# Kernel tuning notes

Hardware: AMD Instinct MI355X
Metric: run time of the kernel (lower is better)

The kernel has to match this reference:

```python
import jax, jax.numpy as jnp
import numpy as np

# Reversible solver constants (init kwargs / solve args)
L = 0.999          # coupling parameter l
H = 1.0 / 64.0     # step size h
T_END = 1.0        # terminal time T
N_STEPS = int(T_END / H)  # 64 sequential steps

B, D, HID = 4096, 512, 2048


def setup_inputs() -> dict:
    key = jax.random.key(0)
    k0, k1, k2, k3 = jax.random.split(key, 4)
    s1 = 1.0 / np.sqrt(D).astype(np.float32)
    s2 = 1.0 / np.sqrt(HID).astype(np.float32)
    return {
        "y0": jax.random.normal(k0, (B, D), jnp.float32),
        "W1": jax.random.normal(k1, (D, HID), jnp.float32) * s1,
        "b1": jnp.zeros((HID,), jnp.float32),
        "wt": jax.random.normal(k2, (HID,), jnp.float32) * 0.1,
        "W2": jax.random.normal(k3, (HID, D), jnp.float32) * s2,
        "b2": jnp.zeros((D,), jnp.float32),
    }


def reference(y0, W1, b1, wt, W2, b2):
    # MLP vector field vf(t, y): [B, D] -> [B, D]
    def vf(t, y):
        hidden = jnp.tanh(y @ W1 + b1 + t * wt)  # [B, HID]
        return hidden @ W2 + b2                   # [B, D]

    # Explicit Euler solver step: step(vf, h, t, y) = h * vf(t, y)
    def euler_step(hh, t, y):
        return hh * vf(t, y)

    # Reversible forward step (faithful to _solve_forward.forward_step)
    def forward_step(carry, _):
        t0, y0_, z0 = carry
        t1 = t0 + H
        y1 = L * y0_ + (1.0 - L) * z0 + euler_step(H, t0, z0)
        z1 = z0 - euler_step(-H, t1, y1)
        return (t1, y1, z1), None

    t0 = jnp.zeros((), jnp.float32)
    (tN, yN, zN), _ = jax.lax.scan(forward_step, (t0, y0, y0), None, length=N_STEPS)
    return yN
```

## Files before the change

### kernel.cpp

```cpp
#include <hip/hip_runtime.h>
#include <hip/hip_bf16.h>

typedef __bf16 bf16x8 __attribute__((ext_vector_type(8)));
typedef float f32x4 __attribute__((ext_vector_type(4)));
typedef unsigned short u16;

#define GLD_LDS16(gp, lp) __builtin_amdgcn_global_load_lds( \
    (const __attribute__((address_space(1))) unsigned int*)(gp), \
    (__attribute__((address_space(3))) unsigned int*)(lp), 16, 0, 0)

__device__ __forceinline__ float tanh_fast(float x) {
  float e = __expf(2.0f * x);
  return 1.0f - __fdividef(2.0f, e + 1.0f);
}

__device__ __forceinline__ u16 bf16_rn(float x) {
  union { float f; unsigned u; } v; v.f = x;
  unsigned r = v.u + 0x7fffu + ((v.u >> 16) & 1u);
  return (u16)(r >> 16);
}

template <int BM, int BN, int BK, int K, int MODE, int NTL>
__global__ __launch_bounds__(256, 2)
void gemm_fused(const u16* __restrict__ A, const u16* __restrict__ Bt,
                const float* __restrict__ bias, const float* __restrict__ wt,
                float tval,
                const float* __restrict__ y_in, const float* __restrict__ z_in,
                float* __restrict__ out32, u16* __restrict__ out_bf, int N) {
  constexpr int NS = BK / 64;
  constexpr int WTM = BM / 2, WTN = BN / 2;
  constexpr int FM = WTM / 16, FN = WTN / 16;
  constexpr int ACH = BM * BK * 2 / 1024;
  constexpr int BCH = BN * BK * 2 / 1024;
  constexpr int CPS_A = BM / 8;
  constexpr int CPS_B = BN / 8;
  constexpr int MT = 4096 / BM;
  constexpr int MPX = MT / 8;
  constexpr int NCH = ACH / 4;
  static_assert(ACH / 4 == BCH / 4 || true, "");

  __shared__ u16 As[NS * BM * 64];
  __shared__ u16 Bs[NS * BN * 64];

  const int tid = threadIdx.x;
  const int wave = tid >> 6;
  const int lane = tid & 63;
  const int wm = wave >> 1, wn = wave & 1;
  const int l15 = lane & 15, kg = lane >> 4;

  const int wg = blockIdx.x;
  const int xcd = wg & 7;
  const int j = wg >> 3;
  const int bm0 = (xcd * MPX + j / NTL) * BM;
  const int bn0 = (j % NTL) * BN;

  f32x4 acc[FM][FN];
#pragma unroll
  for (int m = 0; m < FM; ++m)
#pragma unroll
    for (int n = 0; n < FN; ++n) acc[m][n] = (f32x4){0.f, 0.f, 0.f, 0.f};

  const int sr = lane >> 3;
  const int scs = ((lane & 7) ^ sr) * 8;
  const int rsw = (l15 & 7) << 3;

  const u16* Ag = A + (size_t)bm0 * K;
  const u16* Bg = Bt + (size_t)bn0 * K;

  for (int kt = 0; kt < K / BK; ++kt) {
    const u16* Ak = Ag + kt * BK;
    const u16* Bk = Bg + kt * BK;
#pragma unroll
    for (int i = 0; i < NCH; ++i) {
      {
        const int ch = wave + i * 4;
        const int kh = ch / CPS_A;
        const int rg = ch % CPS_A;
        GLD_LDS16(Ak + (size_t)(rg * 8 + sr) * K + kh * 64 + scs,
                  (char*)As + ch * 1024);
      }
      if (i < BCH / 4) {
        const int ch = wave + i * 4;
        const int kh = ch / CPS_B;
        const int rg = ch % CPS_B;
        GLD_LDS16(Bk + (size_t)(rg * 8 + sr) * K + kh * 64 + scs,
                  (char*)Bs + ch * 1024);
      }
    }
    __syncthreads();
#pragma unroll
    for (int ks = 0; ks < 2 * NS; ++ks) {
      const int kh = ks >> 1;
      const int kc = ((ks & 1) * 32 + kg * 8) ^ rsw;
      bf16x8 af[FM], bfr[FN];
#pragma unroll
      for (int m = 0; m < FM; ++m)
        af[m] = *reinterpret_cast<const bf16x8*>(
            &As[(kh * BM + wm * WTM + m * 16 + l15) * 64 + kc]);
#pragma unroll
      for (int n = 0; n < FN; ++n)
        bfr[n] = *reinterpret_cast<const bf16x8*>(
            &Bs[(kh * BN + wn * WTN + n * 16 + l15) * 64 + kc]);
      __builtin_amdgcn_s_setprio(1);
#pragma unroll
      for (int m = 0; m < FM; ++m)
#pragma unroll
        for (int n = 0; n < FN; ++n)
          acc[m][n] =
              __builtin_amdgcn_mfma_f32_16x16x32_bf16(af[m], bfr[n], acc[m][n], 0, 0, 0);
      __builtin_amdgcn_s_setprio(0);
    }
    __syncthreads();
  }

#pragma unroll
  for (int n = 0; n < FN; ++n) {
    const int col = bn0 + wn * WTN + n * 16 + l15;
    const float bv = bias[col];
    const float wv = (MODE == 0) ? wt[col] : 0.f;
#pragma unroll
    for (int m = 0; m < FM; ++m) {
      const int row0 = bm0 + wm * WTM + m * 16 + kg * 4;
      if (MODE == 0) {
#pragma unroll
        for (int r = 0; r < 4; ++r) {
          const size_t idx = (size_t)(row0 + r) * N + col;
          const float x = acc[m][n][r] + bv + tval * wv;
          out_bf[idx] = bf16_rn(tanh_fast(x));
        }
      } else {
        float yv[4], zv[4];
#pragma unroll
        for (int r = 0; r < 4; ++r) {
          const size_t idx = (size_t)(row0 + r) * N + col;
          zv[r] = z_in[idx];
          if (MODE == 1) yv[r] = y_in[idx];
        }
#pragma unroll
        for (int r = 0; r < 4; ++r) {
          const size_t idx = (size_t)(row0 + r) * N + col;
          const float a = acc[m][n][r] + bv;
          const float v = (MODE == 1)
              ? 0.999f * yv[r] + 0.001f * zv[r] + 0.015625f * a
              : zv[r] + 0.015625f * a;
          out32[idx] = v;
          out_bf[idx] = bf16_rn(v);
        }
      }
    }
  }
}

__global__ void transpose_bf16(const float* __restrict__ in, u16* __restrict__ out,
                               int R, int C) {
  __shared__ float tile[32][33];
  const int bx = blockIdx.x * 32;
  const int by = blockIdx.y * 32;
  const int tx = threadIdx.x, ty = threadIdx.y;
#pragma unroll
  for (int i = 0; i < 32; i += 8)
    tile[ty + i][tx] = in[(size_t)(by + ty + i) * C + (bx + tx)];
  __syncthreads();
#pragma unroll
  for (int i = 0; i < 32; i += 8)
    out[(size_t)(bx + ty + i) * R + (by + tx)] = bf16_rn(tile[tx][ty + i]);
}

__global__ void init_state(const float* __restrict__ y0, float* __restrict__ y32,
                           float* __restrict__ z32, u16* __restrict__ zbf, int n) {
  const int i = blockIdx.x * blockDim.x + threadIdx.x;
  if (i < n) {
    const float v = y0[i];
    y32[i] = v;
    z32[i] = v;
    zbf[i] = bf16_rn(v);
  }
}

extern "C" void kernel_launch(void* const* d_in, const int* in_sizes, int n_in,
                              void* d_out, int out_size, void* d_ws, size_t ws_size,
                              hipStream_t stream) {
  const float* y0 = (const float*)d_in[0];
  const float* W1 = (const float*)d_in[1];
  const float* b1 = (const float*)d_in[2];
  const float* wt = (const float*)d_in[3];
  const float* W2 = (const float*)d_in[4];
  const float* b2 = (const float*)d_in[5];

  constexpr int B = 4096, D = 512, HID = 2048, NSTEP = 64;
  constexpr float Hh = 1.0f / 64.0f;

  char* ws = (char*)d_ws;
  u16* W1t = (u16*)ws; ws += (size_t)HID * D * 2;
  u16* W2t = (u16*)ws; ws += (size_t)D * HID * 2;
  u16* hid = (u16*)ws; ws += (size_t)B * HID * 2;
  float* z32 = (float*)ws; ws += (size_t)B * D * 4;
  u16* ybf = (u16*)ws; ws += (size_t)B * D * 2;
  u16* zbf = (u16*)ws; ws += (size_t)B * D * 2;
  float* y32 = (float*)d_out;

  transpose_bf16<<<dim3(HID / 32, D / 32), dim3(32, 8), 0, stream>>>(W1, W1t, D, HID);
  transpose_bf16<<<dim3(D / 32, HID / 32), dim3(32, 8), 0, stream>>>(W2, W2t, HID, D);
  init_state<<<(B * D + 255) / 256, 256, 0, stream>>>(y0, y32, z32, zbf, B * D);

  for (int s = 0; s < NSTEP; ++s) {
    const float t0 = (float)s * Hh;
    const float t1 = (float)(s + 1) * Hh;
    gemm_fused<128, 128, 128, 512, 0, 16><<<512, 256, 0, stream>>>(
        zbf, W1t, b1, wt, t0, nullptr, nullptr, nullptr, hid, HID);
    gemm_fused<64, 64, 256, 2048, 1, 8><<<512, 256, 0, stream>>>(
        hid, W2t, b2, nullptr, 0.f, y32, z32, y32, ybf, D);
    gemm_fused<128, 128, 128, 512, 0, 16><<<512, 256, 0, stream>>>(
        ybf, W1t, b1, wt, t1, nullptr, nullptr, nullptr, hid, HID);
    gemm_fused<64, 64, 256, 2048, 2, 8><<<512, 256, 0, stream>>>(
        hid, W2t, b2, nullptr, 0.f, nullptr, z32, z32, zbf, D);
  }
}
```

Measured before the change: 4.207 ms.

## Pre-pack W2 into MFMA fragment layout and read B directly from global

W2 is now packed once into a layout that matches the MFMA B-fragment order, so each lane loads its 8 bf16 values with one contiguous 16-byte global read. The W2 GEMMs then skip staging B in LDS, and only A is staged, with BK raised to 512. The goal is to free LDS bandwidth and cut the LDS traffic and barriers spent on B. The risk is that B reads now depend on L2/global latency with no software pipelining, and the larger A stage uses more LDS per block, which may lower occupancy.

```diff
diff --git a/kernel.cpp b/kernel.cpp
--- a/kernel.cpp
+++ b/kernel.cpp
@@ -4,6 +4,7 @@
 typedef __bf16 bf16x8 __attribute__((ext_vector_type(8)));
 typedef float f32x4 __attribute__((ext_vector_type(4)));
 typedef unsigned short u16;
+typedef u16 u16x8 __attribute__((ext_vector_type(8)));
 
 #define GLD_LDS16(gp, lp) __builtin_amdgcn_global_load_lds( \
     (const __attribute__((address_space(1))) unsigned int*)(gp), \
@@ -20,13 +21,11 @@
   return (u16)(r >> 16);
 }
 
-template <int BM, int BN, int BK, int K, int MODE, int NTL>
+template <int BM, int BN, int BK, int K, int NTL>
 __global__ __launch_bounds__(256, 2)
-void gemm_fused(const u16* __restrict__ A, const u16* __restrict__ Bt,
-                const float* __restrict__ bias, const float* __restrict__ wt,
-                float tval,
-                const float* __restrict__ y_in, const float* __restrict__ z_in,
-                float* __restrict__ out32, u16* __restrict__ out_bf, int N) {
+void gemm_hidden(const u16* __restrict__ A, const u16* __restrict__ Bt,
+                 const float* __restrict__ bias, const float* __restrict__ wt,
+                 float tval, u16* __restrict__ out_bf, int N) {
   constexpr int NS = BK / 64;
   constexpr int WTM = BM / 2, WTN = BN / 2;
   constexpr int FM = WTM / 16, FN = WTN / 16;
@@ -34,10 +33,8 @@
   constexpr int BCH = BN * BK * 2 / 1024;
   constexpr int CPS_A = BM / 8;
   constexpr int CPS_B = BN / 8;
-  constexpr int MT = 4096 / BM;
-  constexpr int MPX = MT / 8;
+  constexpr int MPX = (4096 / BM) / 8;
   constexpr int NCH = ACH / 4;
-  static_assert(ACH / 4 == BCH / 4 || true, "");
 
   __shared__ u16 As[NS * BM * 64];
   __shared__ u16 Bs[NS * BN * 64];
@@ -116,39 +113,139 @@
 #pragma unroll
   for (int n = 0; n < FN; ++n) {
     const int col = bn0 + wn * WTN + n * 16 + l15;
-    const float bv = bias[col];
-    const float wv = (MODE == 0) ? wt[col] : 0.f;
+    const float bv = bias[col] + tval * wt[col];
 #pragma unroll
     for (int m = 0; m < FM; ++m) {
       const int row0 = bm0 + wm * WTM + m * 16 + kg * 4;
-      if (MODE == 0) {
-#pragma unroll
-        for (int r = 0; r < 4; ++r) {
-          const size_t idx = (size_t)(row0 + r) * N + col;
-          const float x = acc[m][n][r] + bv + tval * wv;
-          out_bf[idx] = bf16_rn(tanh_fast(x));
-        }
-      } else {
-        float yv[4], zv[4];
-#pragma unroll
-        for (int r = 0; r < 4; ++r) {
-          const size_t idx = (size_t)(row0 + r) * N + col;
-          zv[r] = z_in[idx];
-          if (MODE == 1) yv[r] = y_in[idx];
-        }
-#pragma unroll
-        for (int r = 0; r < 4; ++r) {
-          const size_t idx = (size_t)(row0 + r) * N + col;
-          const float a = acc[m][n][r] + bv;
-          const float v = (MODE == 1)
-              ? 0.999f * yv[r] + 0.001f * zv[r] + 0.015625f * a
-              : zv[r] + 0.015625f * a;
-          out32[idx] = v;
-          out_bf[idx] = bf16_rn(v);
-        }
+#pragma unroll
+      for (int r = 0; r < 4; ++r)
+        out_bf[(size_t)(row0 + r) * N + col] =
+            bf16_rn(tanh_fast(acc[m][n][r] + bv));
+    }
+  }
+}
+
+template <int MODE>
+__global__ __launch_bounds__(256, 2)
+void gemm_update(const u16* __restrict__ A, const u16* __restrict__ Bp,
+                 const float* __restrict__ bias,
+                 const float* __restrict__ y_in, const float* __restrict__ z_in,
+                 float* __restrict__ out32, u16* __restrict__ out_bf) {
+  constexpr int BM = 64, BN = 64, BK = 512, K = 2048, N = 512, NTL = 8;
+  constexpr int NS = BK / 64;
+  constexpr int NT = K / BK;
+  constexpr int ACH = BM * BK * 2 / 1024;
+  constexpr int CPS = BM / 8;
+  constexpr int MPX = (4096 / BM) / 8;
+  constexpr int NB = N / 16;
+
+  __shared__ u16 As[NS * BM * 64];
+
+  const int tid = threadIdx.x;
+  const int wave = tid >> 6;
+  const int lane = tid & 63;
+  const int wm = wave >> 1, wn = wave & 1;
+  const int l15 = lane & 15, kg = lane >> 4;
+
+  const int wg = blockIdx.x;
+  const int xcd = wg & 7;
+  const int j = wg >> 3;
+  const int bm0 = (xcd * MPX + j / NTL) * BM;
+  const int bn0 = (j % NTL) * BN;
+
+  f32x4 acc[2][2];
+#pragma unroll
+  for (int m = 0; m < 2; ++m)
+#pragma unroll
+    for (int n = 0; n < 2; ++n) acc[m][n] = (f32x4){0.f, 0.f, 0.f, 0.f};
+
+  const int sr = lane >> 3;
+  const int scs = ((lane & 7) ^ sr) * 8;
+  const int rsw = (l15 & 7) << 3;
+
+  const u16* Ag = A + (size_t)bm0 * K;
+  const u16* Bpw = Bp + ((size_t)(bn0 / 16 + wn * 2) * 64 + lane) * 8;
+
+  for (int kt = 0; kt < NT; ++kt) {
+    const u16* Ak = Ag + (size_t)kt * BK;
+#pragma unroll
+    for (int i = 0; i < ACH / 4; ++i) {
+      const int ch = wave + i * 4;
+      const int kh = ch / CPS;
+      const int rg = ch % CPS;
+      GLD_LDS16(Ak + (size_t)(rg * 8 + sr) * K + kh * 64 + scs,
+                (char*)As + ch * 1024);
+    }
+    __syncthreads();
+#pragma unroll
+    for (int ks = 0; ks < 2 * NS; ++ks) {
+      const int kh = ks >> 1;
+      const int kcA = ((ks & 1) * 32 + kg * 8) ^ rsw;
+      const int kb = kt * (BK / 32) + ks;
+      bf16x8 af[2], bfr[2];
+#pragma unroll
+      for (int m = 0; m < 2; ++m)
+        af[m] = *reinterpret_cast<const bf16x8*>(
+            &As[(kh * BM + wm * 32 + m * 16 + l15) * 64 + kcA]);
+#pragma unroll
+      for (int n = 0; n < 2; ++n)
+        bfr[n] = *reinterpret_cast<const bf16x8*>(
+            Bpw + (size_t)(kb * NB + n) * 512);
+      __builtin_amdgcn_s_setprio(1);
+#pragma unroll
+      for (int m = 0; m < 2; ++m)
+#pragma unroll
+        for (int n = 0; n < 2; ++n)
+          acc[m][n] =
+              __builtin_amdgcn_mfma_f32_16x16x32_bf16(af[m], bfr[n], acc[m][n], 0, 0, 0);
+      __builtin_amdgcn_s_setprio(0);
+    }
+    __syncthreads();
+  }
+
+#pragma unroll
+  for (int n = 0; n < 2; ++n) {
+    const int col = bn0 + wn * 32 + n * 16 + l15;
+    const float bv = bias[col];
+#pragma unroll
+    for (int m = 0; m < 2; ++m) {
+      const int row0 = bm0 + wm * 32 + m * 16 + kg * 4;
+      float yv[4], zv[4];
+#pragma unroll
+      for (int r = 0; r < 4; ++r) {
+        const size_t idx = (size_t)(row0 + r) * N + col;
+        zv[r] = z_in[idx];
+        if (MODE == 1) yv[r] = y_in[idx];
       }
-    }
-  }
+#pragma unroll
+      for (int r = 0; r < 4; ++r) {
+        const size_t idx = (size_t)(row0 + r) * N + col;
+        const float a = acc[m][n][r] + bv;
+        const float v = (MODE == 1)
+            ? 0.999f * yv[r] + 0.001f * zv[r] + 0.015625f * a
+            : zv[r] + 0.015625f * a;
+        out32[idx] = v;
+        out_bf[idx] = bf16_rn(v);
+      }
+    }
+  }
+}
+
+template <int K, int Nn>
+__global__ void pack_w(const float* __restrict__ W, u16* __restrict__ P) {
+  constexpr int NB = Nn / 16;
+  const int t = blockIdx.x * 256 + threadIdx.x;
+  if (t >= (K / 32) * 4 * NB * 16) return;
+  const int l15 = t & 15;
+  const int nb = (t >> 4) % NB;
+  const int kg = (t >> 4) / NB % 4;
+  const int kb = (t >> 4) / NB / 4;
+  const int n = nb * 16 + l15;
+  const int k0 = kb * 32 + kg * 8;
+  u16x8 o;
+#pragma unroll
+  for (int e = 0; e < 8; ++e) o[e] = bf16_rn(W[(size_t)(k0 + e) * Nn + n]);
+  *reinterpret_cast<u16x8*>(&P[((size_t)(kb * NB + nb) * 64 + kg * 16 + l15) * 8]) = o;
 }
 
 __global__ void transpose_bf16(const float* __restrict__ in, u16* __restrict__ out,
@@ -192,7 +289,7 @@
 
   char* ws = (char*)d_ws;
   u16* W1t = (u16*)ws; ws += (size_t)HID * D * 2;
-  u16* W2t = (u16*)ws; ws += (size_t)D * HID * 2;
+  u16* W2p = (u16*)ws; ws += (size_t)D * HID * 2;
   u16* hid = (u16*)ws; ws += (size_t)B * HID * 2;
   float* z32 = (float*)ws; ws += (size_t)B * D * 4;
   u16* ybf = (u16*)ws; ws += (size_t)B * D * 2;
@@ -200,19 +297,17 @@
   float* y32 = (float*)d_out;
 
   transpose_bf16<<<dim3(HID / 32, D / 32), dim3(32, 8), 0, stream>>>(W1, W1t, D, HID);
-  transpose_bf16<<<dim3(D / 32, HID / 32), dim3(32, 8), 0, stream>>>(W2, W2t, HID, D);
+  pack_w<HID, D><<<(HID / 32) * 4 * (D / 16) * 16 / 256, 256, 0, stream>>>(W2, W2p);
   init_state<<<(B * D + 255) / 256, 256, 0, stream>>>(y0, y32, z32, zbf, B * D);
 
   for (int s = 0; s < NSTEP; ++s) {
     const float t0 = (float)s * Hh;
     const float t1 = (float)(s + 1) * Hh;
-    gemm_fused<128, 128, 128, 512, 0, 16><<<512, 256, 0, stream>>>(
-        zbf, W1t, b1, wt, t0, nullptr, nullptr, nullptr, hid, HID);
-    gemm_fused<64, 64, 256, 2048, 1, 8><<<512, 256, 0, stream>>>(
-        hid, W2t, b2, nullptr, 0.f, y32, z32, y32, ybf, D);
-    gemm_fused<128, 128, 128, 512, 0, 16><<<512, 256, 0, stream>>>(
-        ybf, W1t, b1, wt, t1, nullptr, nullptr, nullptr, hid, HID);
-    gemm_fused<64, 64, 256, 2048, 2, 8><<<512, 256, 0, stream>>>(
-        hid, W2t, b2, nullptr, 0.f, nullptr, z32, z32, zbf, D);
-  }
-}
+    gemm_hidden<128, 128, 128, 512, 16><<<512, 256, 0, stream>>>(
+        zbf, W1t, b1, wt, t0, hid, HID);
+    gemm_update<1><<<512, 256, 0, stream>>>(hid, W2p, b2, y32, z32, y32, ybf);
+    gemm_hidden<128, 128, 128, 512, 16><<<512, 256, 0, stream>>>(
+        ybf, W1t, b1, wt, t1, hid, HID);
+    gemm_update<2><<<512, 256, 0, stream>>>(hid, W2p, b2, nullptr, z32, z32, zbf);
+  }
+}
```

Result: slower. 5.705 ms (+35.6%).
